# Kernel optimization log

Hardware: AMD Instinct MI355X
Metric: run time of the kernel (lower is better)

The kernel has to match this reference:

```python
import jax, jax.numpy as jnp
import numpy as np

N_NODES = 50000
N_EDGES = 800000
IN_CH = 256
HID = 256
OUT_CH = 128


def setup_inputs() -> dict:
    key = jax.random.key(0)
    ks = jax.random.split(key, 12)
    x = jax.random.normal(ks[0], (N_NODES, IN_CH), dtype=jnp.float32)
    adj_rows = jnp.sort(jax.random.randint(ks[1], (N_EDGES,), 0, N_NODES, dtype=jnp.int32))
    adj_cols = jax.random.randint(ks[2], (N_EDGES,), 0, N_NODES, dtype=jnp.int32)
    # normalized adjacency weights (~1/degree scale)
    adj_vals = jax.random.uniform(ks[3], (N_EDGES,), dtype=jnp.float32) / 16.0
    def xavier(k, fan_in, fan_out):
        lim = float(np.sqrt(6.0 / (fan_in + fan_out)))
        return jax.random.uniform(k, (fan_in, fan_out), dtype=jnp.float32, minval=-lim, maxval=lim)
    Wa0 = xavier(ks[4], IN_CH, HID)
    Wa1 = xavier(ks[5], HID, HID)
    Wl0 = xavier(ks[6], IN_CH + HID, HID)
    Wl1 = xavier(ks[7], 2 * HID, OUT_CH)
    return {
        'x': x, 'adj_rows': adj_rows, 'adj_cols': adj_cols, 'adj_vals': adj_vals,
        'Wa0': Wa0, 'ba0': jnp.zeros((HID,), jnp.float32),
        'Wa1': Wa1, 'ba1': jnp.zeros((HID,), jnp.float32),
        'Wl0': Wl0, 'bl0': jnp.zeros((HID,), jnp.float32),
        'Wl1': Wl1, 'bl1': jnp.zeros((OUT_CH,), jnp.float32),
    }


def reference(x, adj_rows, adj_cols, adj_vals, Wa0, ba0, Wa1, ba1, Wl0, bl0, Wl1, bl1):
    n = x.shape[0]

    def spmm(h):
        # sparse adj @ h : gather neighbor rows, scale by edge weight, segment-sum into dst
        return jax.ops.segment_sum(adj_vals[:, None] * h[adj_cols], adj_rows, num_segments=n)

    # layer 0
    agg = jax.nn.relu(spmm(x) @ Wa0 + ba0)
    h = jax.nn.relu(jnp.concatenate((x, agg), axis=1) @ Wl0 + bl0)
    # layer 1 (last: no activation after linear)
    agg = jax.nn.relu(spmm(h) @ Wa1 + ba1)
    h = jnp.concatenate((h, agg), axis=1) @ Wl1 + bl1
    # F.normalize: row-wise L2 with eps=1e-12
    norm = jnp.maximum(jnp.linalg.norm(h, axis=1, keepdims=True), 1e-12)
    return h / norm
```

## Files before the change

kernel.cpp:

```cpp
#include <hip/hip_runtime.h>

typedef unsigned short u16;
typedef __attribute__((ext_vector_type(8))) __bf16 bf16x8;
typedef __attribute__((ext_vector_type(4))) float f32x4;
typedef __attribute__((ext_vector_type(8))) u16 u16x8;
typedef __attribute__((ext_vector_type(4))) u16 u16x4;

__device__ __forceinline__ float bf2f(u16 u) {
  return __builtin_bit_cast(float, ((unsigned)u) << 16);
}
__device__ __forceinline__ u16 f2bf(float f) {
  unsigned x = __builtin_bit_cast(unsigned, f);
  x += 0x7fffu + ((x >> 16) & 1u);
  return (u16)(x >> 16);
}
__device__ __forceinline__ f32x4 cvt4(u16x4 v) {
  return (f32x4){bf2f(v.x), bf2f(v.y), bf2f(v.z), bf2f(v.w)};
}
__device__ __forceinline__ void gload_lds16(const void* g, void* l) {
  __builtin_amdgcn_global_load_lds(
      (const __attribute__((address_space(1))) void*)g,
      (__attribute__((address_space(3))) void*)l, 16, 0, 0);
}

__global__ void prep_kernel(const float* __restrict__ x, u16* __restrict__ x_bf, int cvtxBlocks,
                            const float* __restrict__ W0, u16* __restrict__ T0,
                            const float* __restrict__ W1, u16* __restrict__ T1,
                            const float* __restrict__ W2, u16* __restrict__ T2,
                            const float* __restrict__ W3, u16* __restrict__ T3,
                            const int* __restrict__ rows, int nE, int* __restrict__ rp, int nN) {
  int b = blockIdx.x;
  if (b < cvtxBlocks) {
    int i = b * 256 + threadIdx.x;
    if (i >= nN * 64) return;
    const float4 v = ((const float4*)x)[i];
    u16x4 o = { f2bf(v.x), f2bf(v.y), f2bf(v.z), f2bf(v.w) };
    ((u16x4*)x_bf)[i] = o;
    return;
  }
  b -= cvtxBlocks;
  if (b < 1280) {
    int i = b * 256 + threadIdx.x;
    const float* W; u16* T; int K, N;
    if (i < 65536)        { W = W0; T = T0; K = 256; N = 256; }
    else if (i < 131072)  { W = W1; T = T1; K = 256; N = 256; i -= 65536; }
    else if (i < 262144)  { W = W2; T = T2; K = 512; N = 256; i -= 131072; }
    else if (i < 327680)  { W = W3; T = T3; K = 512; N = 128; i -= 262144; }
    else return;
    int k = i / N, n = i - k * N;
    T[(size_t)n * K + k] = f2bf(W[i]);
    return;
  }
  b -= 1280;
  int i = b * 256 + threadIdx.x;
  if (i > nN) return;
  int lo = 0, hi = nE;
  while (lo < hi) { int mid = (lo + hi) >> 1; if (rows[mid] < i) lo = mid + 1; else hi = mid; }
  rp[i] = lo;
}

__global__ __launch_bounds__(128) void spmm_kernel(
    const u16* __restrict__ X, const int* __restrict__ rp,
    const int* __restrict__ cols, const float* __restrict__ vals,
    u16* __restrict__ out, int nN) {
  int lane = threadIdx.x & 63;
  int node = blockIdx.x * 2 + (threadIdx.x >> 6);
  if (node >= nN) return;
  int e0 = rp[node], e1 = rp[node + 1];
  f32x4 s0 = {0.f, 0.f, 0.f, 0.f}, s1 = s0, s2 = s0, s3 = s0;
  const u16* xp = X + (size_t)lane * 4;
  int e = e0;
  for (; e + 8 <= e1; e += 8) {
    int c[8]; float v[8]; u16x4 xv[8];
    #pragma unroll
    for (int i = 0; i < 8; ++i) { c[i] = cols[e + i]; v[i] = vals[e + i]; }
    #pragma unroll
    for (int i = 0; i < 8; ++i) xv[i] = *(const u16x4*)(xp + (size_t)c[i] * 256);
    s0 += v[0] * cvt4(xv[0]); s1 += v[1] * cvt4(xv[1]);
    s2 += v[2] * cvt4(xv[2]); s3 += v[3] * cvt4(xv[3]);
    s0 += v[4] * cvt4(xv[4]); s1 += v[5] * cvt4(xv[5]);
    s2 += v[6] * cvt4(xv[6]); s3 += v[7] * cvt4(xv[7]);
  }
  if (e + 4 <= e1) {
    int c0 = cols[e], c1 = cols[e + 1], c2 = cols[e + 2], c3 = cols[e + 3];
    float v0 = vals[e], v1 = vals[e + 1], v2 = vals[e + 2], v3 = vals[e + 3];
    u16x4 x0 = *(const u16x4*)(xp + (size_t)c0 * 256);
    u16x4 x1 = *(const u16x4*)(xp + (size_t)c1 * 256);
    u16x4 x2 = *(const u16x4*)(xp + (size_t)c2 * 256);
    u16x4 x3 = *(const u16x4*)(xp + (size_t)c3 * 256);
    s0 += v0 * cvt4(x0); s1 += v1 * cvt4(x1);
    s2 += v2 * cvt4(x2); s3 += v3 * cvt4(x3);
    e += 4;
  }
  for (; e < e1; ++e) {
    int c = cols[e];
    float v = vals[e];
    s0 += v * cvt4(*(const u16x4*)(xp + (size_t)c * 256));
  }
  f32x4 s = (s0 + s1) + (s2 + s3);
  u16x4 o = { f2bf(s.x), f2bf(s.y), f2bf(s.z), f2bf(s.w) };
  *(u16x4*)(out + (size_t)node * 256 + lane * 4) = o;
}

template<int N2, bool NORM>
__global__ __launch_bounds__(256) void fused_kernel(
    const u16* __restrict__ agg, const u16* __restrict__ xh,
    const u16* __restrict__ W1t, const float* __restrict__ b1,
    const u16* __restrict__ W2t, const float* __restrict__ b2,
    void* __restrict__ outp, int M) {
  constexpr int NI2 = N2 / 32;
  __shared__ u16 As[64 * 64];
  __shared__ u16 Bs[256 * 64];
  __shared__ u16 Ag[64 * 256];
  __shared__ float red[64][2];

  const int tid = threadIdx.x;
  const int lane = tid & 63;
  const int wid = tid >> 6;
  const int wr = wid >> 1, wc = wid & 1;
  const int row0b = blockIdx.x * 64;
  const int lr = lane & 15, kg = lane >> 4;

  auto stageA = [&](const u16* src, int kt) {
    #pragma unroll
    for (int i = 0; i < 2; ++i) {
      const int u = i * 256 + tid;
      const int row = u >> 3;
      const int kss = (u & 7) ^ (row & 7);
      int grow = row0b + row; if (grow >= M) grow = M - 1;
      gload_lds16(src + (size_t)grow * 256 + kt * 64 + kss * 8, &As[u * 8]);
    }
  };
  auto stageB = [&](const u16* Wt, int KW, int NC, int kt) {
    const int chunks = NC * 8;
    for (int i = 0; i < chunks / 256; ++i) {
      const int u = i * 256 + tid;
      const int col = u >> 3;
      const int kss = (u & 7) ^ (col & 7);
      gload_lds16(Wt + (size_t)col * KW + kt * 64 + kss * 8, &Bs[u * 8]);
    }
  };

  f32x4 acc[2][8];

  #pragma unroll
  for (int ni = 0; ni < 8; ++ni) {
    float bv = b1[wc * 128 + ni * 16 + lr];
    acc[0][ni] = (f32x4){bv, bv, bv, bv};
    acc[1][ni] = acc[0][ni];
  }
  for (int kt = 0; kt < 4; ++kt) {
    if (kt) __syncthreads();
    stageB(W1t, 256, 256, kt);
    stageA(agg, kt);
    __syncthreads();
    #pragma unroll
    for (int ks = 0; ks < 2; ++ks) {
      const int q = ks * 4 + kg;
      bf16x8 a[2], b[8];
      #pragma unroll
      for (int mi = 0; mi < 2; ++mi) {
        const int r = wr * 32 + mi * 16 + lr;
        a[mi] = __builtin_bit_cast(bf16x8,
            *(const u16x8*)&As[r * 64 + ((q ^ (r & 7)) << 3)]);
      }
      #pragma unroll
      for (int ni = 0; ni < 8; ++ni) {
        const int cb = wc * 128 + ni * 16 + lr;
        b[ni] = __builtin_bit_cast(bf16x8,
            *(const u16x8*)&Bs[cb * 64 + ((q ^ (cb & 7)) << 3)]);
      }
      #pragma unroll
      for (int mi = 0; mi < 2; ++mi)
        #pragma unroll
        for (int ni = 0; ni < 8; ++ni)
          acc[mi][ni] = __builtin_amdgcn_mfma_f32_16x16x32_bf16(a[mi], b[ni], acc[mi][ni], 0, 0, 0);
    }
  }
  #pragma unroll
  for (int mi = 0; mi < 2; ++mi)
    #pragma unroll
    for (int j = 0; j < 4; ++j) {
      const int rl = wr * 32 + mi * 16 + kg * 4 + j;
      #pragma unroll
      for (int ni = 0; ni < 8; ++ni) {
        float v = acc[mi][ni][j];
        v = v > 0.f ? v : 0.f;
        const int c = wc * 128 + ni * 16 + lr;
        Ag[rl * 256 + (c >> 6) * 64 + ((((c >> 3) & 7) ^ (rl & 7)) << 3) + (c & 7)] = f2bf(v);
      }
    }
  __syncthreads();

  #pragma unroll
  for (int ni = 0; ni < NI2; ++ni) {
    float bv = b2[wc * (N2 / 2) + ni * 16 + lr];
    acc[0][ni] = (f32x4){bv, bv, bv, bv};
    acc[1][ni] = acc[0][ni];
  }
  for (int kt = 0; kt < 8; ++kt) {
    if (kt) __syncthreads();
    stageB(W2t, 512, N2, kt);
    if (kt < 4) stageA(xh, kt);
    __syncthreads();
    #pragma unroll
    for (int ks = 0; ks < 2; ++ks) {
      const int q = ks * 4 + kg;
      bf16x8 a[2], b[NI2];
      if (kt < 4) {
        #pragma unroll
        for (int mi = 0; mi < 2; ++mi) {
          const int r = wr * 32 + mi * 16 + lr;
          a[mi] = __builtin_bit_cast(bf16x8,
              *(const u16x8*)&As[r * 64 + ((q ^ (r & 7)) << 3)]);
        }
      } else {
        const int w = kt - 4;
        #pragma unroll
        for (int mi = 0; mi < 2; ++mi) {
          const int r = wr * 32 + mi * 16 + lr;
          a[mi] = __builtin_bit_cast(bf16x8,
              *(const u16x8*)&Ag[r * 256 + w * 64 + ((q ^ (r & 7)) << 3)]);
        }
      }
      #pragma unroll
      for (int ni = 0; ni < NI2; ++ni) {
        const int cb = wc * (N2 / 2) + ni * 16 + lr;
        b[ni] = __builtin_bit_cast(bf16x8,
            *(const u16x8*)&Bs[cb * 64 + ((q ^ (cb & 7)) << 3)]);
      }
      #pragma unroll
      for (int mi = 0; mi < 2; ++mi)
        #pragma unroll
        for (int ni = 0; ni < NI2; ++ni)
          acc[mi][ni] = __builtin_amdgcn_mfma_f32_16x16x32_bf16(a[mi], b[ni], acc[mi][ni], 0, 0, 0);
    }
  }

  float invn[2][4];
  if (NORM) {
    #pragma unroll
    for (int mi = 0; mi < 2; ++mi)
      #pragma unroll
      for (int j = 0; j < 4; ++j) {
        float p = 0.f;
        #pragma unroll
        for (int ni = 0; ni < NI2; ++ni) { float v = acc[mi][ni][j]; p += v * v; }
        #pragma unroll
        for (int m = 1; m < 16; m <<= 1) p += __shfl_xor(p, m, 64);
        int rl = wr * 32 + mi * 16 + kg * 4 + j;
        if (lr == 0) red[rl][wc] = p;
      }
    __syncthreads();
    #pragma unroll
    for (int mi = 0; mi < 2; ++mi)
      #pragma unroll
      for (int j = 0; j < 4; ++j) {
        int rl = wr * 32 + mi * 16 + kg * 4 + j;
        float ss = red[rl][0] + red[rl][1];
        float nrm = sqrtf(ss);
        nrm = nrm > 1e-12f ? nrm : 1e-12f;
        invn[mi][j] = 1.f / nrm;
      }
  }

  #pragma unroll
  for (int mi = 0; mi < 2; ++mi)
    #pragma unroll
    for (int j = 0; j < 4; ++j) {
      int r = row0b + wr * 32 + mi * 16 + kg * 4 + j;
      if (r >= M) continue;
      #pragma unroll
      for (int ni = 0; ni < NI2; ++ni) {
        float v = acc[mi][ni][j];
        int c = wc * (N2 / 2) + ni * 16 + lr;
        if (NORM) {
          ((float*)outp)[(size_t)r * N2 + c] = v * invn[mi][j];
        } else {
          v = v > 0.f ? v : 0.f;
          ((u16*)outp)[(size_t)r * N2 + c] = f2bf(v);
        }
      }
    }
}

extern "C" void kernel_launch(void* const* d_in, const int* in_sizes, int n_in,
                              void* d_out, int out_size, void* d_ws, size_t ws_size,
                              hipStream_t stream) {
  const float* x        = (const float*)d_in[0];
  const int*   adj_rows = (const int*)d_in[1];
  const int*   adj_cols = (const int*)d_in[2];
  const float* adj_vals = (const float*)d_in[3];
  const float* Wa0 = (const float*)d_in[4];
  const float* ba0 = (const float*)d_in[5];
  const float* Wa1 = (const float*)d_in[6];
  const float* ba1 = (const float*)d_in[7];
  const float* Wl0 = (const float*)d_in[8];
  const float* bl0 = (const float*)d_in[9];
  const float* Wl1 = (const float*)d_in[10];
  const float* bl1 = (const float*)d_in[11];

  const int nN = in_sizes[0] / 256;
  const int nE = in_sizes[1];

  char* ws = (char*)d_ws;
  size_t off = 0;
  auto alloc = [&](size_t bytes) -> void* {
    void* p = ws + off;
    off += (bytes + 255) & ~(size_t)255;
    return p;
  };
  u16* x_bf  = (u16*)alloc((size_t)nN * 256 * 2);
  u16* aggA  = (u16*)alloc((size_t)nN * 256 * 2);
  u16* h_bf  = (u16*)alloc((size_t)nN * 256 * 2);
  int* rp    = (int*)alloc((size_t)(nN + 1) * 4);
  u16* wt_a0 = (u16*)alloc(256 * 256 * 2);
  u16* wt_a1 = (u16*)alloc(256 * 256 * 2);
  u16* wt_l0 = (u16*)alloc(512 * 256 * 2);
  u16* wt_l1 = (u16*)alloc(512 * 128 * 2);
  if (off > ws_size) return;

  dim3 blk(256);
  const int cvtxBlocks = (nN * 64 + 255) / 256;
  const int rpBlocks = (nN + 1 + 255) / 256;
  prep_kernel<<<dim3(cvtxBlocks + 1280 + rpBlocks), blk, 0, stream>>>(
      x, x_bf, cvtxBlocks, Wa0, wt_a0, Wa1, wt_a1, Wl0, wt_l0, Wl1, wt_l1,
      adj_rows, nE, rp, nN);

  const int MB = (nN + 63) / 64;
  dim3 gF(MB);
  dim3 gNode((nN + 1) / 2);
  dim3 sblk(128);

  spmm_kernel<<<gNode, sblk, 0, stream>>>(x_bf, rp, adj_cols, adj_vals, aggA, nN);
  fused_kernel<256, false><<<gF, blk, 0, stream>>>(aggA, x_bf, wt_a0, ba0, wt_l0, bl0, h_bf, nN);
  spmm_kernel<<<gNode, sblk, 0, stream>>>(h_bf, rp, adj_cols, adj_vals, aggA, nN);
  fused_kernel<128, true><<<gF, blk, 0, stream>>>(aggA, h_bf, wt_a1, ba1, wt_l1, bl1, (float*)d_out, nN);
}
```

Measured before the change: 199.9 us.

## Fuse SpMM gather into the GEMM kernel, aggregating directly into shared memory

The separate SpMM kernel is removed. Each 64-row GEMM block now computes its own neighbor aggregation straight into the LDS Ag tile, and the first GEMM reads its A operand from that tile instead of staging it from a global agg buffer. This drops a global write and read of the aggregation buffer plus two kernel launches. In exchange the gather phase runs at the GEMM kernel's occupancy (256 threads with large LDS), with each wave serially handling 16 nodes, which may hide gather latency less well than the dedicated 128-thread kernel did.

```diff
diff --git a/kernel.cpp b/kernel.cpp
--- a/kernel.cpp
+++ b/kernel.cpp
@@ -59,52 +59,10 @@
   rp[i] = lo;
 }
 
-__global__ __launch_bounds__(128) void spmm_kernel(
-    const u16* __restrict__ X, const int* __restrict__ rp,
+template<int N2, bool NORM>
+__global__ __launch_bounds__(256) void mega_kernel(
+    const u16* __restrict__ Xg, const int* __restrict__ rp,
     const int* __restrict__ cols, const float* __restrict__ vals,
-    u16* __restrict__ out, int nN) {
-  int lane = threadIdx.x & 63;
-  int node = blockIdx.x * 2 + (threadIdx.x >> 6);
-  if (node >= nN) return;
-  int e0 = rp[node], e1 = rp[node + 1];
-  f32x4 s0 = {0.f, 0.f, 0.f, 0.f}, s1 = s0, s2 = s0, s3 = s0;
-  const u16* xp = X + (size_t)lane * 4;
-  int e = e0;
-  for (; e + 8 <= e1; e += 8) {
-    int c[8]; float v[8]; u16x4 xv[8];
-    #pragma unroll
-    for (int i = 0; i < 8; ++i) { c[i] = cols[e + i]; v[i] = vals[e + i]; }
-    #pragma unroll
-    for (int i = 0; i < 8; ++i) xv[i] = *(const u16x4*)(xp + (size_t)c[i] * 256);
-    s0 += v[0] * cvt4(xv[0]); s1 += v[1] * cvt4(xv[1]);
-    s2 += v[2] * cvt4(xv[2]); s3 += v[3] * cvt4(xv[3]);
-    s0 += v[4] * cvt4(xv[4]); s1 += v[5] * cvt4(xv[5]);
-    s2 += v[6] * cvt4(xv[6]); s3 += v[7] * cvt4(xv[7]);
-  }
-  if (e + 4 <= e1) {
-    int c0 = cols[e], c1 = cols[e + 1], c2 = cols[e + 2], c3 = cols[e + 3];
-    float v0 = vals[e], v1 = vals[e + 1], v2 = vals[e + 2], v3 = vals[e + 3];
-    u16x4 x0 = *(const u16x4*)(xp + (size_t)c0 * 256);
-    u16x4 x1 = *(const u16x4*)(xp + (size_t)c1 * 256);
-    u16x4 x2 = *(const u16x4*)(xp + (size_t)c2 * 256);
-    u16x4 x3 = *(const u16x4*)(xp + (size_t)c3 * 256);
-    s0 += v0 * cvt4(x0); s1 += v1 * cvt4(x1);
-    s2 += v2 * cvt4(x2); s3 += v3 * cvt4(x3);
-    e += 4;
-  }
-  for (; e < e1; ++e) {
-    int c = cols[e];
-    float v = vals[e];
-    s0 += v * cvt4(*(const u16x4*)(xp + (size_t)c * 256));
-  }
-  f32x4 s = (s0 + s1) + (s2 + s3);
-  u16x4 o = { f2bf(s.x), f2bf(s.y), f2bf(s.z), f2bf(s.w) };
-  *(u16x4*)(out + (size_t)node * 256 + lane * 4) = o;
-}
-
-template<int N2, bool NORM>
-__global__ __launch_bounds__(256) void fused_kernel(
-    const u16* __restrict__ agg, const u16* __restrict__ xh,
     const u16* __restrict__ W1t, const float* __restrict__ b1,
     const u16* __restrict__ W2t, const float* __restrict__ b2,
     void* __restrict__ outp, int M) {
@@ -121,6 +79,46 @@
   const int row0b = blockIdx.x * 64;
   const int lr = lane & 15, kg = lane >> 4;
 
+  {
+    const u16* xp = Xg + (size_t)lane * 4;
+    const int c = lane * 4;
+    const int agoff = (c >> 6) * 64 + (c & 7);
+    for (int t = 0; t < 16; ++t) {
+      const int rl = wid * 16 + t;
+      const int node = row0b + rl;
+      if (node >= M) break;
+      int e0 = rp[node], e1 = rp[node + 1];
+      f32x4 s0 = {0.f, 0.f, 0.f, 0.f}, s1 = s0, s2 = s0, s3 = s0;
+      int e = e0;
+      for (; e + 8 <= e1; e += 8) {
+        int cc[8]; float v[8]; u16x4 xv[8];
+        #pragma unroll
+        for (int i = 0; i < 8; ++i) { cc[i] = cols[e + i]; v[i] = vals[e + i]; }
+        #pragma unroll
+        for (int i = 0; i < 8; ++i) xv[i] = *(const u16x4*)(xp + (size_t)cc[i] * 256);
+        s0 += v[0] * cvt4(xv[0]); s1 += v[1] * cvt4(xv[1]);
+        s2 += v[2] * cvt4(xv[2]); s3 += v[3] * cvt4(xv[3]);
+        s0 += v[4] * cvt4(xv[4]); s1 += v[5] * cvt4(xv[5]);
+        s2 += v[6] * cvt4(xv[6]); s3 += v[7] * cvt4(xv[7]);
+      }
+      if (e + 4 <= e1) {
+        int c0 = cols[e], c1 = cols[e + 1], c2 = cols[e + 2], c3 = cols[e + 3];
+        float v0 = vals[e], v1 = vals[e + 1], v2 = vals[e + 2], v3 = vals[e + 3];
+        s0 += v0 * cvt4(*(const u16x4*)(xp + (size_t)c0 * 256));
+        s1 += v1 * cvt4(*(const u16x4*)(xp + (size_t)c1 * 256));
+        s2 += v2 * cvt4(*(const u16x4*)(xp + (size_t)c2 * 256));
+        s3 += v3 * cvt4(*(const u16x4*)(xp + (size_t)c3 * 256));
+        e += 4;
+      }
+      for (; e < e1; ++e)
+        s0 += vals[e] * cvt4(*(const u16x4*)(xp + (size_t)cols[e] * 256));
+      f32x4 s = (s0 + s1) + (s2 + s3);
+      u16x4 o = { f2bf(s.x), f2bf(s.y), f2bf(s.z), f2bf(s.w) };
+      *(u16x4*)&Ag[rl * 256 + agoff + ((((c >> 3) & 7) ^ (rl & 7)) << 3)] = o;
+    }
+  }
+  __syncthreads();
+
   auto stageA = [&](const u16* src, int kt) {
     #pragma unroll
     for (int i = 0; i < 2; ++i) {
@@ -152,7 +150,6 @@
   for (int kt = 0; kt < 4; ++kt) {
     if (kt) __syncthreads();
     stageB(W1t, 256, 256, kt);
-    stageA(agg, kt);
     __syncthreads();
     #pragma unroll
     for (int ks = 0; ks < 2; ++ks) {
@@ -162,7 +159,7 @@
       for (int mi = 0; mi < 2; ++mi) {
         const int r = wr * 32 + mi * 16 + lr;
         a[mi] = __builtin_bit_cast(bf16x8,
-            *(const u16x8*)&As[r * 64 + ((q ^ (r & 7)) << 3)]);
+            *(const u16x8*)&Ag[r * 256 + kt * 64 + ((q ^ (r & 7)) << 3)]);
       }
       #pragma unroll
       for (int ni = 0; ni < 8; ++ni) {
@@ -177,6 +174,8 @@
           acc[mi][ni] = __builtin_amdgcn_mfma_f32_16x16x32_bf16(a[mi], b[ni], acc[mi][ni], 0, 0, 0);
     }
   }
+  __syncthreads();
+
   #pragma unroll
   for (int mi = 0; mi < 2; ++mi)
     #pragma unroll
@@ -201,7 +200,7 @@
   for (int kt = 0; kt < 8; ++kt) {
     if (kt) __syncthreads();
     stageB(W2t, 512, N2, kt);
-    if (kt < 4) stageA(xh, kt);
+    if (kt < 4) stageA(Xg, kt);
     __syncthreads();
     #pragma unroll
     for (int ks = 0; ks < 2; ++ks) {
@@ -311,7 +310,6 @@
     return p;
   };
   u16* x_bf  = (u16*)alloc((size_t)nN * 256 * 2);
-  u16* aggA  = (u16*)alloc((size_t)nN * 256 * 2);
   u16* h_bf  = (u16*)alloc((size_t)nN * 256 * 2);
   int* rp    = (int*)alloc((size_t)(nN + 1) * 4);
   u16* wt_a0 = (u16*)alloc(256 * 256 * 2);
@@ -329,11 +327,9 @@
 
   const int MB = (nN + 63) / 64;
   dim3 gF(MB);
-  dim3 gNode((nN + 1) / 2);
-  dim3 sblk(128);
-
-  spmm_kernel<<<gNode, sblk, 0, stream>>>(x_bf, rp, adj_cols, adj_vals, aggA, nN);
-  fused_kernel<256, false><<<gF, blk, 0, stream>>>(aggA, x_bf, wt_a0, ba0, wt_l0, bl0, h_bf, nN);
-  spmm_kernel<<<gNode, sblk, 0, stream>>>(h_bf, rp, adj_cols, adj_vals, aggA, nN);
-  fused_kernel<128, true><<<gF, blk, 0, stream>>>(aggA, h_bf, wt_a1, ba1, wt_l1, bl1, (float*)d_out, nN);
-}
+
+  mega_kernel<256, false><<<gF, blk, 0, stream>>>(
+      x_bf, rp, adj_cols, adj_vals, wt_a0, ba0, wt_l0, bl0, h_bf, nN);
+  mega_kernel<128, true><<<gF, blk, 0, stream>>>(
+      h_bf, rp, adj_cols, adj_vals, wt_a1, ba1, wt_l1, bl1, (float*)d_out, nN);
+}
```

Result: slower. 291.4 us (+45.8%).
